# Kernel tuning notes

Hardware: AMD Instinct MI355X
Metric: run time of the kernel (lower is better)

## Reference

```python
import jax, jax.numpy as jnp
import numpy as np

BLOCK = 64  # bitsandbytes 4-bit blocksize
OUT, IN = 4096, 4096
# NF4 codebook (bitsandbytes values)
NF4_CODE = np.array([
    -1.0, -0.6961928009986877, -0.5250730514526367, -0.39491748809814453,
    -0.28444138169288635, -0.18477343022823334, -0.09105003625154495, 0.0,
    0.07958029955625534, 0.16093020141124725, 0.24611230194568634,
    0.33791524171829224, 0.44070982933044434, 0.5626170039176941,
    0.7229568362236023, 1.0], dtype=np.float32)


def setup_inputs() -> dict:
    key = jax.random.key(0)
    k1, k2, k3 = jax.random.split(key, 3)
    x = jax.random.normal(k1, (8, 2048, IN), dtype=jnp.float32)
    qweight = jax.random.randint(k2, (OUT * IN,), 0, 16, dtype=jnp.int32)
    absmax = jax.random.uniform(k3, (OUT * IN // BLOCK,), dtype=jnp.float32)
    return {"x": x, "qweight": qweight, "absmax": absmax}


def reference(x, qweight, absmax):
    code = jnp.asarray(NF4_CODE)
    # dequantize: codebook lookup, then per-block absmax scaling
    w = code[qweight].reshape(-1, BLOCK) * absmax[:, None]  # [n_blocks, BLOCK]
    W = w.reshape(OUT, IN)                                   # [out, in]
    # linear: y = x @ W^T  (no bias: quantized_bias is None)
    return jnp.einsum('bsi,oi->bso', x, W)
```

## Files before the change

kernel.cpp:

```cpp
#include <hip/hip_runtime.h>
#include <hip/hip_bf16.h>
#include <stdint.h>

#define IN_DIM  4096
#define OUT_DIM 4096
#define M_DIM   16384

#define BM 128
#define BN 128
#define BK 64
#define TM_TILES (M_DIM / BM)
#define TN_TILES (OUT_DIM / BN)

typedef float f32x4 __attribute__((ext_vector_type(4)));
typedef short bf16x8 __attribute__((ext_vector_type(8)));
typedef short bf16x4 __attribute__((ext_vector_type(4)));
typedef int   i32x4 __attribute__((ext_vector_type(4)));

__device__ __constant__ float NF4_CODE_D[16] = {
    -1.0f, -0.6961928009986877f, -0.5250730514526367f, -0.39491748809814453f,
    -0.28444138169288635f, -0.18477343022823334f, -0.09105003625154495f, 0.0f,
    0.07958029955625534f, 0.16093020141124725f, 0.24611230194568634f,
    0.33791524171829224f, 0.44070982933044434f, 0.5626170039176941f,
    0.7229568362236023f, 1.0f};

static __device__ __forceinline__ ushort f2bf(float f) {
  union { float f; uint32_t u; } v; v.f = f;
  uint32_t r = v.u + 0x7FFFu + ((v.u >> 16) & 1u);
  return (ushort)(r >> 16);
}

__global__ void dequant_nf4(const int* __restrict__ q, const float* __restrict__ am,
                            ushort* __restrict__ w) {
  __shared__ float code[16];
  if (threadIdx.x < 16) code[threadIdx.x] = NF4_CODE_D[threadIdx.x];
  __syncthreads();
  size_t t = (size_t)blockIdx.x * blockDim.x + threadIdx.x;
  size_t base = t * 8;
  i32x4 qa = *(const i32x4*)(q + base);
  i32x4 qb = *(const i32x4*)(q + base + 4);
  float s = am[base >> 6];
  bf16x8 o;
  o[0] = (short)f2bf(code[qa[0] & 15] * s);
  o[1] = (short)f2bf(code[qa[1] & 15] * s);
  o[2] = (short)f2bf(code[qa[2] & 15] * s);
  o[3] = (short)f2bf(code[qa[3] & 15] * s);
  o[4] = (short)f2bf(code[qb[0] & 15] * s);
  o[5] = (short)f2bf(code[qb[1] & 15] * s);
  o[6] = (short)f2bf(code[qb[2] & 15] * s);
  o[7] = (short)f2bf(code[qb[3] & 15] * s);
  *(bf16x8*)(w + base) = o;
}

__global__ void cvt_x(const float* __restrict__ x, ushort* __restrict__ xb) {
  size_t t = (size_t)blockIdx.x * blockDim.x + threadIdx.x;
  size_t base = t * 8;
  f32x4 a = *(const f32x4*)(x + base);
  f32x4 b = *(const f32x4*)(x + base + 4);
  bf16x8 o;
  o[0] = (short)f2bf(a[0]); o[1] = (short)f2bf(a[1]);
  o[2] = (short)f2bf(a[2]); o[3] = (short)f2bf(a[3]);
  o[4] = (short)f2bf(b[0]); o[5] = (short)f2bf(b[1]);
  o[6] = (short)f2bf(b[2]); o[7] = (short)f2bf(b[3]);
  *(bf16x8*)(xb + base) = o;
}

static __device__ __forceinline__ void llds16(const ushort* g, ushort* l) {
  __builtin_amdgcn_global_load_lds(
      (const __attribute__((address_space(1))) void*)g,
      (__attribute__((address_space(3))) void*)l, 16, 0, 0);
}

template<bool XBF>
__global__ void gemm_k(const float* __restrict__ X, const ushort* __restrict__ Xb,
                       const ushort* __restrict__ W, float* __restrict__ Y) {
  __shared__ ushort As[BM * BK];
  __shared__ ushort Bs[BN * BK];

  const int tid  = threadIdx.x;
  const int lane = tid & 63;
  const int wid  = tid >> 6;
  const int wr   = wid >> 1;
  const int wc   = wid & 1;

  const int nwg = TM_TILES * TN_TILES;
  const int cpx = nwg >> 3;
  const int bid = blockIdx.x;
  const int wg  = (bid & 7) * cpx + (bid >> 3);
  const int tm  = wg / TN_TILES;
  const int tn  = wg % TN_TILES;

  const size_t row0 = (size_t)tm * BM;
  const size_t col0 = (size_t)tn * BN;

  f32x4 acc[4][4] = {};

  const int arow = lane & 15;
  const int kgrp = lane >> 4;

  const int srow = lane >> 3;
  const int scol = (lane & 7) * 8;

  for (int k0 = 0; k0 < IN_DIM; k0 += BK) {
    if (XBF) {
#pragma unroll
      for (int i = 0; i < 4; ++i) {
        const int c = wid * 4 + i;
        llds16(Xb + (row0 + c * 8 + srow) * IN_DIM + k0 + scol, As + c * 512);
      }
    } else {
      f32x4 r[8];
#pragma unroll
      for (int i = 0; i < 8; ++i) {
        const int row = i * 16 + (tid >> 4);
        const int col = (tid & 15) * 4;
        r[i] = *(const f32x4*)(X + (row0 + row) * IN_DIM + k0 + col);
      }
#pragma unroll
      for (int i = 0; i < 8; ++i) {
        const int row = i * 16 + (tid >> 4);
        const int col = (tid & 15) * 4;
        bf16x4 o;
        o[0] = (short)f2bf(r[i][0]); o[1] = (short)f2bf(r[i][1]);
        o[2] = (short)f2bf(r[i][2]); o[3] = (short)f2bf(r[i][3]);
        *(bf16x4*)&As[row * BK + col] = o;
      }
    }
#pragma unroll
    for (int i = 0; i < 4; ++i) {
      const int c = wid * 4 + i;
      llds16(W + (col0 + c * 8 + srow) * IN_DIM + k0 + scol, Bs + c * 512);
    }
    __syncthreads();

#pragma unroll
    for (int ks = 0; ks < 2; ++ks) {
      bf16x8 a[4], b[4];
#pragma unroll
      for (int m = 0; m < 4; ++m)
        a[m] = *(const bf16x8*)&As[(wr * 64 + m * 16 + arow) * BK + ks * 32 + kgrp * 8];
#pragma unroll
      for (int n = 0; n < 4; ++n)
        b[n] = *(const bf16x8*)&Bs[(wc * 64 + n * 16 + arow) * BK + ks * 32 + kgrp * 8];
#pragma unroll
      for (int m = 0; m < 4; ++m)
#pragma unroll
        for (int n = 0; n < 4; ++n)
          acc[m][n] = __builtin_amdgcn_mfma_f32_16x16x32_bf16(a[m], b[n], acc[m][n], 0, 0, 0);
    }
    __syncthreads();
  }

  float* yb = Y + (row0 + wr * 64) * OUT_DIM + col0 + wc * 64;
  const int crow = (lane >> 4) * 4;
  const int ccol = lane & 15;
#pragma unroll
  for (int m = 0; m < 4; ++m)
#pragma unroll
    for (int n = 0; n < 4; ++n)
#pragma unroll
      for (int v = 0; v < 4; ++v)
        yb[(size_t)(m * 16 + crow + v) * OUT_DIM + n * 16 + ccol] = acc[m][n][v];
}

extern "C" void kernel_launch(void* const* d_in, const int* in_sizes, int n_in,
                              void* d_out, int out_size, void* d_ws, size_t ws_size,
                              hipStream_t stream) {
  const float* x  = (const float*)d_in[0];
  const int*   q  = (const int*)d_in[1];
  const float* am = (const float*)d_in[2];
  float* y = (float*)d_out;

  ushort* w = (ushort*)d_ws;
  const size_t WB = (size_t)OUT_DIM * IN_DIM * sizeof(ushort);
  const size_t XB = (size_t)M_DIM * IN_DIM * sizeof(ushort);

  dequant_nf4<<<(OUT_DIM * (size_t)IN_DIM) / 8 / 256, 256, 0, stream>>>(q, am, w);

  const int ngrid = TM_TILES * TN_TILES;
  if (ws_size >= WB + XB) {
    ushort* xb = (ushort*)((char*)d_ws + WB);
    cvt_x<<<((size_t)M_DIM * IN_DIM) / 8 / 256, 256, 0, stream>>>(x, xb);
    gemm_k<true><<<ngrid, 256, 0, stream>>>(x, xb, w, y);
  } else {
    gemm_k<false><<<ngrid, 256, 0, stream>>>(x, nullptr, w, y);
  }
}
```

Before: 721.5 us.

## Replace GEMM with 256x256 double-buffered, swizzled, pipelined 8-wave kernel

The main bf16 GEMM moves from 128x128 tiles with 4 waves to 256x256 tiles with 8 waves. LDS is double-buffered, and global-to-LDS loads for the next k-tile are interleaved with MFMA quads using manual barriers, vmcnt waits and s_setprio. LDS columns are XOR-swizzled to avoid bank conflicts. The goal is more data reuse per tile and hiding of load latency behind compute. The cost is 128KB of LDS and much higher register pressure, and a fragile hand-scheduled barrier and wait sequence.

```diff
diff --git a/kernel.cpp b/kernel.cpp
--- a/kernel.cpp
+++ b/kernel.cpp
@@ -5,12 +5,8 @@
 #define IN_DIM  4096
 #define OUT_DIM 4096
 #define M_DIM   16384
-
-#define BM 128
-#define BN 128
-#define BK 64
-#define TM_TILES (M_DIM / BM)
-#define TN_TILES (OUT_DIM / BN)
+#define BK      64
+#define NT      (IN_DIM / BK)
 
 typedef float f32x4 __attribute__((ext_vector_type(4)));
 typedef short bf16x8 __attribute__((ext_vector_type(8)));
@@ -71,77 +67,170 @@
       (__attribute__((address_space(3))) void*)l, 16, 0, 0);
 }
 
-template<bool XBF>
-__global__ void gemm_k(const float* __restrict__ X, const ushort* __restrict__ Xb,
-                       const ushort* __restrict__ W, float* __restrict__ Y) {
-  __shared__ ushort As[BM * BK];
-  __shared__ ushort Bs[BN * BK];
+__global__ __launch_bounds__(512, 2) void gemm256(const ushort* __restrict__ Xb,
+                                                  const ushort* __restrict__ W,
+                                                  float* __restrict__ Y) {
+  __shared__ ushort As[2][256 * BK];
+  __shared__ ushort Bs[2][256 * BK];
 
   const int tid  = threadIdx.x;
   const int lane = tid & 63;
   const int wid  = tid >> 6;
-  const int wr   = wid >> 1;
-  const int wc   = wid & 1;
-
-  const int nwg = TM_TILES * TN_TILES;
-  const int cpx = nwg >> 3;
+  const int wr   = wid >> 2;
+  const int wc   = wid & 3;
+  const int l15  = lane & 15;
+  const int kg   = lane >> 4;
+  const int l7   = lane & 7;
+
   const int bid = blockIdx.x;
-  const int wg  = (bid & 7) * cpx + (bid >> 3);
-  const int tm  = wg / TN_TILES;
-  const int tn  = wg % TN_TILES;
-
-  const size_t row0 = (size_t)tm * BM;
-  const size_t col0 = (size_t)tn * BN;
-
+  const int wg  = (bid & 7) * 128 + (bid >> 3);
+  const int tm  = wg >> 4;
+  const int tn  = wg & 15;
+  const size_t row0 = (size_t)tm * 256;
+  const size_t col0 = (size_t)tn * 256;
+
+  const int srow  = tid >> 3;
+  const int scol8 = ((tid & 7) ^ (srow & 7)) * 8;
+  const int wbase = wid << 9;
+
+  f32x4  acc[8][4] = {};
+  bf16x8 a[4][2], b0[2][2], b1[2][2];
+
+#define BARX()  asm volatile("s_barrier" ::: "memory")
+#define VMC4()  asm volatile("s_waitcnt vmcnt(4)" ::: "memory")
+#define VMC0()  asm volatile("s_waitcnt vmcnt(0)" ::: "memory")
+#define PRI1()  __builtin_amdgcn_s_setprio(1)
+#define PRI0()  __builtin_amdgcn_s_setprio(0)
+
+#define STAGE_A(kt, h, nb) do { \
+    llds16(Xb + (row0 + (h)*128 +  0 + srow) * IN_DIM + (kt)*BK + scol8, \
+           &As[nb][(h)*8192 +    0 + wbase]); \
+    llds16(Xb + (row0 + (h)*128 + 64 + srow) * IN_DIM + (kt)*BK + scol8, \
+           &As[nb][(h)*8192 + 4096 + wbase]); \
+  } while (0)
+
+#define STAGE_B(kt, h, nb) do { \
+    llds16(W + (col0 + (h)*128 +  0 + srow) * IN_DIM + (kt)*BK + scol8, \
+           &Bs[nb][(h)*8192 +    0 + wbase]); \
+    llds16(W + (col0 + (h)*128 + 64 + srow) * IN_DIM + (kt)*BK + scol8, \
+           &Bs[nb][(h)*8192 + 4096 + wbase]); \
+  } while (0)
+
+#define LDA(nb, mh) do { \
+    _Pragma("unroll") for (int mi = 0; mi < 4; ++mi) \
+    _Pragma("unroll") for (int ks = 0; ks < 2; ++ks) \
+      a[mi][ks] = *(const bf16x8*)&As[nb][(wr*128 + (mh)*64 + mi*16 + l15) * BK \
+                                          + (((ks*4 + kg) ^ l7) * 8)]; \
+  } while (0)
+
+#define LDB(nb, nh, bb) do { \
+    _Pragma("unroll") for (int ni = 0; ni < 2; ++ni) \
+    _Pragma("unroll") for (int ks = 0; ks < 2; ++ks) \
+      bb[ni][ks] = *(const bf16x8*)&Bs[nb][(wc*64 + (nh)*32 + ni*16 + l15) * BK \
+                                           + (((ks*4 + kg) ^ l7) * 8)]; \
+  } while (0)
+
+#define QUAD(mh, nh, bb) do { \
+    _Pragma("unroll") for (int mi = 0; mi < 4; ++mi) \
+    _Pragma("unroll") for (int ni = 0; ni < 2; ++ni) \
+    _Pragma("unroll") for (int ks = 0; ks < 2; ++ks) \
+      acc[(mh)*4 + mi][(nh)*2 + ni] = __builtin_amdgcn_mfma_f32_16x16x32_bf16( \
+          a[mi][ks], bb[ni][ks], acc[(mh)*4 + mi][(nh)*2 + ni], 0, 0, 0); \
+  } while (0)
+
+#define KTILE(cur, tA, tB) do { \
+    LDA(cur, 0); LDB(cur, 0, b0); STAGE_A(tA, 0, (cur)^1); \
+    BARX(); PRI1(); QUAD(0, 0, b0); PRI0(); BARX(); \
+    LDB(cur, 1, b1); STAGE_A(tA, 1, (cur)^1); \
+    BARX(); PRI1(); QUAD(0, 1, b1); PRI0(); BARX(); \
+    LDA(cur, 1); STAGE_B(tB, 0, cur); \
+    BARX(); PRI1(); QUAD(1, 1, b1); PRI0(); BARX(); \
+    STAGE_B(tB, 1, cur); \
+    BARX(); PRI1(); QUAD(1, 0, b0); PRI0(); VMC4(); BARX(); \
+  } while (0)
+
+  STAGE_B(0, 0, 0); STAGE_B(0, 1, 0);
+  STAGE_A(0, 0, 0); STAGE_A(0, 1, 0);
+  STAGE_B(1, 0, 1); STAGE_B(1, 1, 1);
+  VMC4(); BARX();
+
+#pragma unroll 1
+  for (int t = 0; t < NT - 3; t += 2) {
+    KTILE(0, t + 1, t + 2);
+    KTILE(1, t + 2, t + 3);
+  }
+
+  LDA(0, 0); LDB(0, 0, b0); STAGE_A(NT - 1, 0, 1);
+  BARX(); PRI1(); QUAD(0, 0, b0); PRI0(); BARX();
+  LDB(0, 1, b1); STAGE_A(NT - 1, 1, 1);
+  BARX(); PRI1(); QUAD(0, 1, b1); PRI0(); BARX();
+  LDA(0, 1);
+  BARX(); PRI1(); QUAD(1, 1, b1); PRI0(); BARX();
+  BARX(); PRI1(); QUAD(1, 0, b0); PRI0(); VMC0(); BARX();
+
+  LDA(1, 0); LDB(1, 0, b0); LDB(1, 1, b1);
+  QUAD(0, 0, b0); QUAD(0, 1, b1);
+  LDA(1, 1);
+  QUAD(1, 1, b1); QUAD(1, 0, b0);
+
+#undef KTILE
+#undef QUAD
+#undef LDB
+#undef LDA
+#undef STAGE_B
+#undef STAGE_A
+
+  float* yb = Y + (row0 + wr * 128 + kg * 4) * OUT_DIM + col0 + wc * 64 + l15;
+#pragma unroll
+  for (int m = 0; m < 8; ++m)
+#pragma unroll
+    for (int n = 0; n < 4; ++n)
+#pragma unroll
+      for (int v = 0; v < 4; ++v)
+        yb[(size_t)(m * 16 + v) * OUT_DIM + n * 16] = acc[m][n][v];
+}
+
+__global__ void gemm_fb(const float* __restrict__ X, const ushort* __restrict__ W,
+                        float* __restrict__ Y) {
+  __shared__ ushort Af[128 * 64];
+  __shared__ ushort Bf[128 * 64];
+  const int tid  = threadIdx.x;
+  const int lane = tid & 63;
+  const int wid  = tid >> 6;
+  const int wr   = wid >> 1, wc = wid & 1;
+  const int bid  = blockIdx.x;
+  const int tm   = bid / 32, tn = bid % 32;
+  const size_t row0 = (size_t)tm * 128, col0 = (size_t)tn * 128;
   f32x4 acc[4][4] = {};
-
-  const int arow = lane & 15;
-  const int kgrp = lane >> 4;
-
-  const int srow = lane >> 3;
-  const int scol = (lane & 7) * 8;
-
-  for (int k0 = 0; k0 < IN_DIM; k0 += BK) {
-    if (XBF) {
-#pragma unroll
-      for (int i = 0; i < 4; ++i) {
-        const int c = wid * 4 + i;
-        llds16(Xb + (row0 + c * 8 + srow) * IN_DIM + k0 + scol, As + c * 512);
-      }
-    } else {
-      f32x4 r[8];
-#pragma unroll
-      for (int i = 0; i < 8; ++i) {
-        const int row = i * 16 + (tid >> 4);
-        const int col = (tid & 15) * 4;
-        r[i] = *(const f32x4*)(X + (row0 + row) * IN_DIM + k0 + col);
-      }
-#pragma unroll
-      for (int i = 0; i < 8; ++i) {
-        const int row = i * 16 + (tid >> 4);
-        const int col = (tid & 15) * 4;
-        bf16x4 o;
-        o[0] = (short)f2bf(r[i][0]); o[1] = (short)f2bf(r[i][1]);
-        o[2] = (short)f2bf(r[i][2]); o[3] = (short)f2bf(r[i][3]);
-        *(bf16x4*)&As[row * BK + col] = o;
-      }
+  const int arow = lane & 15, kgrp = lane >> 4;
+  const int srow = lane >> 3, scol = (lane & 7) * 8;
+  for (int k0 = 0; k0 < IN_DIM; k0 += 64) {
+    f32x4 r[8];
+#pragma unroll
+    for (int i = 0; i < 8; ++i)
+      r[i] = *(const f32x4*)(X + (row0 + i * 16 + (tid >> 4)) * IN_DIM + k0 + (tid & 15) * 4);
+#pragma unroll
+    for (int i = 0; i < 8; ++i) {
+      bf16x4 o;
+      o[0] = (short)f2bf(r[i][0]); o[1] = (short)f2bf(r[i][1]);
+      o[2] = (short)f2bf(r[i][2]); o[3] = (short)f2bf(r[i][3]);
+      *(bf16x4*)&Af[(i * 16 + (tid >> 4)) * 64 + (tid & 15) * 4] = o;
     }
 #pragma unroll
     for (int i = 0; i < 4; ++i) {
       const int c = wid * 4 + i;
-      llds16(W + (col0 + c * 8 + srow) * IN_DIM + k0 + scol, Bs + c * 512);
+      llds16(W + (col0 + c * 8 + srow) * IN_DIM + k0 + scol, Bf + c * 512);
     }
     __syncthreads();
-
 #pragma unroll
     for (int ks = 0; ks < 2; ++ks) {
       bf16x8 a[4], b[4];
 #pragma unroll
       for (int m = 0; m < 4; ++m)
-        a[m] = *(const bf16x8*)&As[(wr * 64 + m * 16 + arow) * BK + ks * 32 + kgrp * 8];
+        a[m] = *(const bf16x8*)&Af[(wr * 64 + m * 16 + arow) * 64 + ks * 32 + kgrp * 8];
 #pragma unroll
       for (int n = 0; n < 4; ++n)
-        b[n] = *(const bf16x8*)&Bs[(wc * 64 + n * 16 + arow) * BK + ks * 32 + kgrp * 8];
+        b[n] = *(const bf16x8*)&Bf[(wc * 64 + n * 16 + arow) * 64 + ks * 32 + kgrp * 8];
 #pragma unroll
       for (int m = 0; m < 4; ++m)
 #pragma unroll
@@ -150,10 +239,8 @@
     }
     __syncthreads();
   }
-
   float* yb = Y + (row0 + wr * 64) * OUT_DIM + col0 + wc * 64;
-  const int crow = (lane >> 4) * 4;
-  const int ccol = lane & 15;
+  const int crow = (lane >> 4) * 4, ccol = lane & 15;
 #pragma unroll
   for (int m = 0; m < 4; ++m)
 #pragma unroll
@@ -177,12 +264,11 @@
 
   dequant_nf4<<<(OUT_DIM * (size_t)IN_DIM) / 8 / 256, 256, 0, stream>>>(q, am, w);
 
-  const int ngrid = TM_TILES * TN_TILES;
   if (ws_size >= WB + XB) {
     ushort* xb = (ushort*)((char*)d_ws + WB);
     cvt_x<<<((size_t)M_DIM * IN_DIM) / 8 / 256, 256, 0, stream>>>(x, xb);
-    gemm_k<true><<<ngrid, 256, 0, stream>>>(x, xb, w, y);
+    gemm256<<<(M_DIM / 256) * (OUT_DIM / 256), 512, 0, stream>>>(xb, w, y);
   } else {
-    gemm_k<false><<<ngrid, 256, 0, stream>>>(x, nullptr, w, y);
+    gemm_fb<<<(M_DIM / 128) * (OUT_DIM / 128), 256, 0, stream>>>(x, w, y);
   }
 }
```

Result: faster. 633.6 us (-12.2%).
